# Kernel optimization log

Measured on AMD Instinct MI355X. Metric: run time of the kernel, lower is better.

The kernel has to match this reference:

```python
import jax, jax.numpy as jnp
import numpy as np

NUM_HEADS = 12


def _rel_indices(H, W):
    # [N, N, 3] with channels (dx, dy, dx^2+dy^2), N = H*W
    indx = jnp.arange(W)[None, :] - jnp.arange(W)[:, None]          # [W, W]
    indx = jnp.tile(indx, (H, H))                                    # [N, N]
    indy = jnp.arange(H)[None, :] - jnp.arange(H)[:, None]          # [H, H]
    indy = jnp.repeat(jnp.repeat(indy, W, axis=0), W, axis=1)        # [N, N]
    indd = indx ** 2 + indy ** 2
    return jnp.stack([indx, indy, indd], axis=-1).astype(jnp.float32)


def setup_inputs() -> dict:
    key = jax.random.key(0)
    ks = jax.random.split(key, 8)
    B, N, C = 16, 576, 768
    std = 0.02
    return {
        "x": jax.random.normal(ks[0], (B, N, C), dtype=jnp.float32),
        "Wq": jax.random.normal(ks[1], (C, C), dtype=jnp.float32) * std,
        "Wk": jax.random.normal(ks[2], (C, C), dtype=jnp.float32) * std,
        "Wv": jax.random.normal(ks[3], (C, C), dtype=jnp.float32) * std,
        "Wproj": jax.random.normal(ks[4], (C, C), dtype=jnp.float32) * std,
        "bproj": jnp.zeros((C,), dtype=jnp.float32),
        "pos_w": jax.random.normal(ks[5], (3, NUM_HEADS), dtype=jnp.float32) * std,
        "pos_b": jnp.zeros((NUM_HEADS,), dtype=jnp.float32),
        "gating": jnp.ones((NUM_HEADS,), dtype=jnp.float32),
        "H": 24,
        "W": 24,
    }


def reference(x, Wq, Wk, Wv, Wproj, bproj, pos_w, pos_b, gating, H, W):
    B, N, C = x.shape
    h = gating.shape[0]
    d = C // h
    scale = d ** (-0.5)

    def heads(t):  # [B,N,C] -> [B,h,N,d]
        return t.reshape(B, N, h, d).transpose(0, 2, 1, 3)

    q = heads(x @ Wq)
    k = heads(x @ Wk)
    v = heads(x @ Wv)

    # content scores: [B,h,N,N]
    patch_score = jax.nn.softmax(jnp.einsum('bhnd,bhmd->bhnm', q, k) * scale, axis=-1)

    # positional scores: shared across batch, [h,N,N]
    rel = _rel_indices(H, W)                      # [N,N,3]
    pos_score = jnp.einsum('nmc,ch->hnm', rel, pos_w) + pos_b[:, None, None]
    pos_score = jax.nn.softmax(pos_score, axis=-1)

    gate = jax.nn.sigmoid(gating)[None, :, None, None]  # [1,h,1,1]
    attn = (1.0 - gate) * patch_score + gate * pos_score[None]
    attn = attn / jnp.sum(attn, axis=-1, keepdims=True)

    out = jnp.einsum('bhnm,bhmd->bhnd', attn, v)         # [B,h,N,d]
    out = out.transpose(0, 2, 1, 3).reshape(B, N, C)
    return out @ Wproj + bproj
```

## Files before the change

### kernel.cpp

```cpp
#include <hip/hip_runtime.h>
#include <math.h>

#define B_ 16
#define N_ 576
#define C_ 768
#define NH 12
#define D_ 64
#define GW 24
#define STR 68
#define QKV 2304

typedef unsigned short u16;
typedef __bf16 bf16x8 __attribute__((ext_vector_type(8)));
typedef float f32x4 __attribute__((ext_vector_type(4)));

__device__ __forceinline__ u16 f2bf(float f) {
    unsigned u = __builtin_bit_cast(unsigned, f);
    unsigned r = (u + 0x7FFFu + ((u >> 16) & 1u)) >> 16;
    return (u16)r;
}
__device__ __forceinline__ float bf2f(u16 b) {
    unsigned u = ((unsigned)b) << 16;
    return __builtin_bit_cast(float, u);
}

__device__ __forceinline__ bf16x8 ldsF8u(const u16* p) {
    union { uint2 u[2]; bf16x8 v; } t;
    t.u[0] = *(const uint2*)p;
    t.u[1] = *(const uint2*)(p + 4);
    return t.v;
}
__device__ __forceinline__ bf16x8 ldsF8a(const u16* p) {
    union { uint4 u; bf16x8 v; } t;
    t.u = *(const uint4*)p;
    return t.v;
}

__device__ __forceinline__ void gload16(const u16* g, u16* l) {
    __builtin_amdgcn_global_load_lds(
        (const __attribute__((address_space(1))) void*)g,
        (__attribute__((address_space(3))) void*)l,
        16, 0, 0);
}

__global__ __launch_bounds__(256)
void conv_x_kernel(const float* __restrict__ x, u16* __restrict__ xb)
{
    int i = blockIdx.x * 256 + threadIdx.x;
    float4 v = ((const float4*)x)[i];
    u16 o[4] = {f2bf(v.x), f2bf(v.y), f2bf(v.z), f2bf(v.w)};
    *(uint2*)&xb[(size_t)i * 4] = *(const uint2*)o;
}

__global__ __launch_bounds__(256)
void transpose_w4_kernel(const float* __restrict__ w0, const float* __restrict__ w1,
                         const float* __restrict__ w2, const float* __restrict__ w3,
                         u16* __restrict__ dst_base)
{
    const float* srcs[4] = {w0, w1, w2, w3};
    const float* src = srcs[blockIdx.z];
    u16* dst = dst_base + (size_t)blockIdx.z * C_ * C_;
    __shared__ float t[32][33];
    const int bx = blockIdx.x * 32, by = blockIdx.y * 32;
    const int tx = threadIdx.x & 31, ty = threadIdx.x >> 5;
#pragma unroll
    for (int i = 0; i < 32; i += 8)
        t[ty + i][tx] = src[(size_t)(by + ty + i) * C_ + bx + tx];
    __syncthreads();
#pragma unroll
    for (int i = 0; i < 32; i += 8)
        dst[(size_t)(bx + ty + i) * C_ + by + tx] = f2bf(t[tx][ty + i]);
}

__global__ __launch_bounds__(256)
void transpose_v_kernel(const u16* __restrict__ qkvb, u16* __restrict__ vtb)
{
    __shared__ u16 t[64 * 72];
    const int n0 = blockIdx.x * 64;
    const int bh = blockIdx.y;
    const int b = bh / NH, h = bh % NH;
    const int tid = threadIdx.x;
    const u16* src = qkvb + ((size_t)b * N_ + n0) * QKV + 2 * C_ + h * D_;
#pragma unroll
    for (int p = 0; p < 2; ++p) {
        int idx = p * 256 + tid;
        int r = idx >> 3, c = (idx & 7) << 3;
        *(uint4*)&t[r * 72 + c] = *(const uint4*)(src + (size_t)r * QKV + c);
    }
    __syncthreads();
    u16* dst = vtb + (size_t)bh * D_ * N_ + n0;
#pragma unroll
    for (int p = 0; p < 2; ++p) {
        int idx = p * 256 + tid;
        int dd = idx >> 3, n8 = (idx & 7) << 3;
        u16 o[8];
#pragma unroll
        for (int j = 0; j < 8; ++j) o[j] = t[(n8 + j) * 72 + dd];
        *(uint4*)(dst + (size_t)dd * N_ + n8) = *(const uint4*)o;
    }
}

__global__ __launch_bounds__(256)
void mfma_gemm(const u16* __restrict__ A,
               const u16* __restrict__ BT,
               const float* __restrict__ bias,
               float* __restrict__ out,
               u16* __restrict__ outb,
               int ldo, int mode)
{
    const int K = C_;
    __shared__ __align__(16) u16 As[128 * 64];
    __shared__ __align__(16) u16 Bs[128 * 64];
    const int tid = threadIdx.x;
    const int wave = tid >> 6, lane = tid & 63;
    const int quad = lane >> 4, l16 = lane & 15;
    const int wy = wave >> 1, wx = wave & 1;
    const int tm = blockIdx.y * 128, tn = blockIdx.x * 128;

    const int lr = lane >> 3;
    const int sc = ((lane & 7) ^ lr) * 8;

    f32x4 acc[4][4];
#pragma unroll
    for (int i = 0; i < 4; ++i)
#pragma unroll
        for (int j = 0; j < 4; ++j)
            acc[i][j] = (f32x4){0.f, 0.f, 0.f, 0.f};

    for (int k0 = 0; k0 < K; k0 += 64) {
        __syncthreads();
#pragma unroll
        for (int t = 0; t < 4; ++t) {
            const int rg = wave * 32 + t * 8;
            gload16(A  + (size_t)(tm + rg + lr) * K + k0 + sc, &As[rg * 64]);
            gload16(BT + (size_t)(tn + rg + lr) * K + k0 + sc, &Bs[rg * 64]);
        }
        __syncthreads();

#pragma unroll
        for (int kh = 0; kh < 2; ++kh) {
            bf16x8 aA[4], bB[4];
#pragma unroll
            for (int i = 0; i < 4; ++i) {
                const int s = (kh * 4 + quad) ^ (l16 & 7);
                aA[i] = ldsF8a(&As[(wy * 64 + i * 16 + l16) * 64 + s * 8]);
            }
#pragma unroll
            for (int j = 0; j < 4; ++j) {
                const int s = (kh * 4 + quad) ^ (l16 & 7);
                bB[j] = ldsF8a(&Bs[(wx * 64 + j * 16 + l16) * 64 + s * 8]);
            }
#pragma unroll
            for (int i = 0; i < 4; ++i)
#pragma unroll
                for (int j = 0; j < 4; ++j)
                    acc[i][j] = __builtin_amdgcn_mfma_f32_16x16x32_bf16(aA[i], bB[j], acc[i][j], 0, 0, 0);
        }
    }

    if (mode == 0) {
#pragma unroll
        for (int i = 0; i < 4; ++i) {
#pragma unroll
            for (int r = 0; r < 4; ++r) {
                const int m = tm + wy * 64 + i * 16 + quad * 4 + r;
#pragma unroll
                for (int j = 0; j < 4; ++j) {
                    const int c = tn + wx * 64 + j * 16 + l16;
                    out[(size_t)m * ldo + c] = acc[i][j][r] + bias[c];
                }
            }
        }
    } else {
        const float scale = (tn < C_) ? 0.125f : 1.0f;
#pragma unroll
        for (int i = 0; i < 4; ++i) {
#pragma unroll
            for (int r = 0; r < 4; ++r) {
                const int m = tm + wy * 64 + i * 16 + quad * 4 + r;
#pragma unroll
                for (int j = 0; j < 4; ++j) {
                    const int c = tn + wx * 64 + j * 16 + l16;
                    outb[(size_t)m * ldo + c] = f2bf(acc[i][j][r] * scale);
                }
            }
        }
    }
}

__global__ __launch_bounds__(256)
void pos_stage1_kernel(const u16* __restrict__ qkvb,
                       const float* __restrict__ pos_w,
                       float* __restrict__ T1)
{
    const int bh = blockIdx.x;
    const int b = bh / NH, h = bh % NH;
    const int tid = threadIdx.x;
    __shared__ float ey[47];
    const float w1 = pos_w[NH + h], w2 = pos_w[2 * NH + h];

    if (tid < 47) {
        float dy = (float)(tid - 23);
        ey[tid] = __expf(w1 * dy + w2 * dy * dy);
    }
    __syncthreads();
    if (tid >= 192) return;
    const int mx = tid >> 3, c = (tid & 7) << 3;
    const u16* src = qkvb + (size_t)b * N_ * QKV + 2 * C_ + h * D_ + c;

#pragma unroll
    for (int np = 0; np < 3; ++np) {
        float acc[8][8];
#pragma unroll
        for (int q = 0; q < 8; ++q)
#pragma unroll
            for (int j = 0; j < 8; ++j) acc[q][j] = 0.f;
        for (int my = 0; my < GW; ++my) {
            union { uint4 u; u16 s[8]; } d;
            d.u = *(const uint4*)(src + (size_t)(my * GW + mx) * QKV);
            float vf[8];
#pragma unroll
            for (int j = 0; j < 8; ++j) vf[j] = bf2f(d.s[j]);
#pragma unroll
            for (int q = 0; q < 8; ++q) {
                float e = ey[my - (np * 8 + q) + 23];
#pragma unroll
                for (int j = 0; j < 8; ++j) acc[q][j] += e * vf[j];
            }
        }
#pragma unroll
        for (int q = 0; q < 8; ++q) {
            const int ny = np * 8 + q;
            float* dst = T1 + (((size_t)bh * GW + ny) * GW + mx) * D_ + c;
            *(float4*)dst       = *(float4*)&acc[q][0];
            *(float4*)(dst + 4) = *(float4*)&acc[q][4];
        }
    }
}

__global__ __launch_bounds__(256)
void pos_stage2_kernel(const float* __restrict__ T1,
                       const float* __restrict__ pos_w,
                       const float* __restrict__ gating,
                       u16* __restrict__ aob)
{
    const int bh = blockIdx.x;
    const int ny = blockIdx.y;
    const int b = bh / NH, h = bh % NH;
    const int tid = threadIdx.x;
    __shared__ float T1s[GW * D_];
    __shared__ float ex[47];
    __shared__ float SxA[GW];
    __shared__ float Sy;
    const float w0 = pos_w[h], w1 = pos_w[NH + h], w2 = pos_w[2 * NH + h];

    const float* tsrc = T1 + ((size_t)bh * GW + ny) * GW * D_;
#pragma unroll
    for (int i = 0; i < 2; ++i) {
        int idx = i * 256 + tid;
        if (idx < 384) ((float4*)T1s)[idx] = ((const float4*)tsrc)[idx];
    }
    if (tid < 47) {
        float dx = (float)(tid - 23);
        ex[tid] = __expf(w0 * dx + w2 * dx * dx);
    }
    if (tid == 192) {
        float s = 0.f;
        for (int my = 0; my < GW; ++my) {
            float dy = (float)(my - ny);
            s += __expf(w1 * dy + w2 * dy * dy);
        }
        Sy = s;
    }
    __syncthreads();
    if (tid < GW) {
        float s = 0.f;
        for (int mx = 0; mx < GW; ++mx) s += ex[mx - tid + 23];
        SxA[tid] = s;
    }
    __syncthreads();
    if (tid >= 192) return;
    const int nx = tid >> 3, c = (tid & 7) << 3;

    float acc[8];
#pragma unroll
    for (int j = 0; j < 8; ++j) acc[j] = 0.f;
    for (int mx = 0; mx < GW; ++mx) {
        float e = ex[mx - nx + 23];
        float4 t0 = *(float4*)&T1s[mx * D_ + c];
        float4 t1 = *(float4*)&T1s[mx * D_ + c + 4];
        acc[0] += e * t0.x; acc[1] += e * t0.y; acc[2] += e * t0.z; acc[3] += e * t0.w;
        acc[4] += e * t1.x; acc[5] += e * t1.y; acc[6] += e * t1.z; acc[7] += e * t1.w;
    }
    const float g = 1.f / (1.f + __expf(-gating[h]));
    const float sc = g / (SxA[nx] * Sy);
    const int n = ny * GW + nx;
    u16* dst = aob + ((size_t)b * N_ + n) * C_ + h * D_ + c;
    u16 cur[8];
    *(uint4*)cur = *(const uint4*)dst;
    u16 o[8];
#pragma unroll
    for (int j = 0; j < 8; ++j) o[j] = f2bf(bf2f(cur[j]) + sc * acc[j]);
    *(uint4*)dst = *(const uint4*)o;
}

__global__ __launch_bounds__(256)
void attn_kernel(const u16* __restrict__ qkvb,
                 const u16* __restrict__ vt,
                 const float* __restrict__ gating,
                 u16* __restrict__ ao)
{
    const int qt = blockIdx.x;
    const int bh = blockIdx.y;
    const int b = bh / NH, h = bh % NH;
    const int tid = threadIdx.x;
    const int wave = tid >> 6, lane = tid & 63;
    const int quad = lane >> 4, l16 = lane & 15;

    __shared__ u16 smem[3 * 64 * STR];
    u16* Kt = smem;
    u16* Vs = smem + 64 * STR;
    u16* Pb = smem + 2 * 64 * STR;

    const u16* qptr  = qkvb + ((size_t)b * N_ + qt * 64) * QKV + h * D_;
    const u16* kbase = qkvb + (size_t)b * N_ * QKV + C_ + h * D_;
    const u16* vbase = vt + (size_t)bh * D_ * N_;

    const int sr = tid >> 3;
    const int scol = (tid & 7) << 3;

#pragma unroll
    for (int p = 0; p < 2; ++p) {
        int r = p * 32 + sr;
        uint4 d = *(const uint4*)(qptr + (size_t)r * QKV + scol);
        *(uint2*)&Pb[r * STR + scol]     = make_uint2(d.x, d.y);
        *(uint2*)&Pb[r * STR + scol + 4] = make_uint2(d.z, d.w);
    }
    __syncthreads();

    const int arow = wave * 16 + l16;
    bf16x8 aq0 = ldsF8u(&Pb[arow * STR + quad * 8]);
    bf16x8 aq1 = ldsF8u(&Pb[arow * STR + 32 + quad * 8]);

    uint4 rk[2], rv[2];
    auto loadT = [&](int m0) {
#pragma unroll
        for (int p = 0; p < 2; ++p) {
            int r = p * 32 + sr;
            rk[p] = *(const uint4*)(kbase + (size_t)(m0 + r) * QKV + scol);
            rv[p] = *(const uint4*)(vbase + (size_t)r * N_ + m0 + scol);
        }
    };
    auto writeT = [&]() {
#pragma unroll
        for (int p = 0; p < 2; ++p) {
            int r = p * 32 + sr;
            *(uint2*)&Kt[r * STR + scol]     = make_uint2(rk[p].x, rk[p].y);
            *(uint2*)&Kt[r * STR + scol + 4] = make_uint2(rk[p].z, rk[p].w);
            *(uint2*)&Vs[r * STR + scol]     = make_uint2(rv[p].x, rv[p].y);
            *(uint2*)&Vs[r * STR + scol + 4] = make_uint2(rv[p].z, rv[p].w);
        }
    };

    loadT(0);

    f32x4 oc[4];
#pragma unroll
    for (int nt = 0; nt < 4; ++nt)
        oc[nt] = (f32x4){0.f, 0.f, 0.f, 0.f};
    float lrun[4] = {0.f, 0.f, 0.f, 0.f};

    for (int mt = 0; mt < 9; ++mt) {
        __syncthreads();
        writeT();
        __syncthreads();
        if (mt < 8) loadT((mt + 1) * 64);

        f32x4 s[4];
#pragma unroll
        for (int nt = 0; nt < 4; ++nt) {
            bf16x8 b0 = ldsF8u(&Kt[(nt * 16 + l16) * STR + quad * 8]);
            bf16x8 b1 = ldsF8u(&Kt[(nt * 16 + l16) * STR + 32 + quad * 8]);
            f32x4 z = (f32x4){0.f, 0.f, 0.f, 0.f};
            z = __builtin_amdgcn_mfma_f32_16x16x32_bf16(aq0, b0, z, 0, 0, 0);
            z = __builtin_amdgcn_mfma_f32_16x16x32_bf16(aq1, b1, z, 0, 0, 0);
            s[nt] = z;
        }

#pragma unroll
        for (int r = 0; r < 4; ++r) {
            const int prow = (wave * 16 + quad * 4 + r) * STR;
            float e0 = __expf(s[0][r]);
            float e1 = __expf(s[1][r]);
            float e2 = __expf(s[2][r]);
            float e3 = __expf(s[3][r]);
            Pb[prow +  0 + l16] = f2bf(e0);
            Pb[prow + 16 + l16] = f2bf(e1);
            Pb[prow + 32 + l16] = f2bf(e2);
            Pb[prow + 48 + l16] = f2bf(e3);
            lrun[r] += (e0 + e1) + (e2 + e3);
        }
        asm volatile("s_waitcnt lgkmcnt(0)" ::: "memory");

#pragma unroll
        for (int ks = 0; ks < 2; ++ks) {
            bf16x8 ap = ldsF8u(&Pb[arow * STR + ks * 32 + quad * 8]);
#pragma unroll
            for (int nt = 0; nt < 4; ++nt) {
                bf16x8 bv = ldsF8u(&Vs[(nt * 16 + l16) * STR + ks * 32 + quad * 8]);
                oc[nt] = __builtin_amdgcn_mfma_f32_16x16x32_bf16(ap, bv, oc[nt], 0, 0, 0);
            }
        }
    }

#pragma unroll
    for (int r = 0; r < 4; ++r) {
        lrun[r] += __shfl_xor(lrun[r], 1, 64);
        lrun[r] += __shfl_xor(lrun[r], 2, 64);
        lrun[r] += __shfl_xor(lrun[r], 4, 64);
        lrun[r] += __shfl_xor(lrun[r], 8, 64);
    }

    const float g = 1.f / (1.f + __expf(-gating[h]));
#pragma unroll
    for (int r = 0; r < 4; ++r) {
        const float sc = (1.f - g) / lrun[r];
        const int row = qt * 64 + wave * 16 + quad * 4 + r;
#pragma unroll
        for (int nt = 0; nt < 4; ++nt) {
            ao[((size_t)b * N_ + row) * C_ + h * D_ + nt * 16 + l16] =
                f2bf(oc[nt][r] * sc);
        }
    }
}

extern "C" void kernel_launch(void* const* d_in, const int* in_sizes, int n_in,
                              void* d_out, int out_size, void* d_ws, size_t ws_size,
                              hipStream_t stream)
{
    const float* x      = (const float*)d_in[0];
    const float* Wq     = (const float*)d_in[1];
    const float* Wk     = (const float*)d_in[2];
    const float* Wv     = (const float*)d_in[3];
    const float* Wproj  = (const float*)d_in[4];
    const float* bproj  = (const float*)d_in[5];
    const float* pos_w  = (const float*)d_in[6];
    const float* gating = (const float*)d_in[8];
    float* out = (float*)d_out;

    const size_t xe = (size_t)B_ * N_ * C_;
    const size_t we = (size_t)C_ * C_;
    const size_t qe = (size_t)B_ * N_ * QKV;
    u16* xb   = (u16*)d_ws;
    u16* wt   = xb + xe;
    u16* qkvb = wt + 4 * we;
    u16* vtb  = qkvb + qe;
    u16* aob  = vtb + xe;
    float* T1 = (float*)(aob + xe);
    size_t need = (size_t)(3 * xe + 4 * we + qe) * sizeof(u16)
                + (size_t)B_ * NH * GW * GW * D_ * sizeof(float);
    if (ws_size < need) return;

    conv_x_kernel<<<dim3((unsigned)(xe / 1024)), 256, 0, stream>>>(x, xb);
    transpose_w4_kernel<<<dim3(24, 24, 4), 256, 0, stream>>>(Wq, Wk, Wv, Wproj, wt);

    mfma_gemm<<<dim3(18, 72), 256, 0, stream>>>(xb, wt, nullptr, nullptr,
                                                qkvb, QKV, 1);
    transpose_v_kernel<<<dim3(9, B_ * NH), 256, 0, stream>>>(qkvb, vtb);
    pos_stage1_kernel<<<dim3(B_ * NH), 256, 0, stream>>>(qkvb, pos_w, T1);
    attn_kernel<<<dim3(9, B_ * NH), 256, 0, stream>>>(qkvb, vtb, gating, aob);
    pos_stage2_kernel<<<dim3(B_ * NH, GW), 256, 0, stream>>>(T1, pos_w, gating, aob);
    mfma_gemm<<<dim3(6, 72), 256, 0, stream>>>(aob, wt + 3 * we, bproj, out,
                                               nullptr, C_, 0);
}
```

Before: 258.1 us.

## Merge prep and V-transpose kernels; vectorize GEMM epilogue via swapped MFMA operands

Folds the x-conversion and weight-transpose kernels into one launch, and the V-transpose and positional stage-1 kernels into another, so there are fewer launches and the independent work can run concurrently. Swaps the MFMA operands so each lane holds four consecutive columns. The fp32 epilogue then writes float4 stores with vector bias loads, and the bf16 epilogue stages through padded LDS for coalesced 16-byte row stores. This adds an extra LDS round-trip and barrier in the bf16 path, and makes the merged kernels heterogeneous.

```diff
diff --git a/kernel.cpp b/kernel.cpp
--- a/kernel.cpp
+++ b/kernel.cpp
@@ -9,6 +9,7 @@
 #define GW 24
 #define STR 68
 #define QKV 2304
+#define CSTR 136
 
 typedef unsigned short u16;
 typedef __bf16 bf16x8 __attribute__((ext_vector_type(8)));
@@ -44,25 +45,29 @@
 }
 
 __global__ __launch_bounds__(256)
-void conv_x_kernel(const float* __restrict__ x, u16* __restrict__ xb)
-{
-    int i = blockIdx.x * 256 + threadIdx.x;
-    float4 v = ((const float4*)x)[i];
-    u16 o[4] = {f2bf(v.x), f2bf(v.y), f2bf(v.z), f2bf(v.w)};
-    *(uint2*)&xb[(size_t)i * 4] = *(const uint2*)o;
-}
-
-__global__ __launch_bounds__(256)
-void transpose_w4_kernel(const float* __restrict__ w0, const float* __restrict__ w1,
-                         const float* __restrict__ w2, const float* __restrict__ w3,
-                         u16* __restrict__ dst_base)
-{
+void prep_kernel(const float* __restrict__ x,
+                 const float* __restrict__ w0, const float* __restrict__ w1,
+                 const float* __restrict__ w2, const float* __restrict__ w3,
+                 u16* __restrict__ xb, u16* __restrict__ wt_base)
+{
+    const int tid = threadIdx.x;
+    if (blockIdx.z == 4) {
+        const int flat = blockIdx.y * 24 + blockIdx.x;
+#pragma unroll
+        for (int it = 0; it < 12; ++it) {
+            int idx = flat * 3072 + it * 256 + tid;
+            float4 v = ((const float4*)x)[idx];
+            u16 o[4] = {f2bf(v.x), f2bf(v.y), f2bf(v.z), f2bf(v.w)};
+            *(uint2*)&xb[(size_t)idx * 4] = *(const uint2*)o;
+        }
+        return;
+    }
     const float* srcs[4] = {w0, w1, w2, w3};
     const float* src = srcs[blockIdx.z];
-    u16* dst = dst_base + (size_t)blockIdx.z * C_ * C_;
+    u16* dst = wt_base + (size_t)blockIdx.z * C_ * C_;
     __shared__ float t[32][33];
     const int bx = blockIdx.x * 32, by = blockIdx.y * 32;
-    const int tx = threadIdx.x & 31, ty = threadIdx.x >> 5;
+    const int tx = tid & 31, ty = tid >> 5;
 #pragma unroll
     for (int i = 0; i < 32; i += 8)
         t[ty + i][tx] = src[(size_t)(by + ty + i) * C_ + bx + tx];
@@ -70,34 +75,6 @@
 #pragma unroll
     for (int i = 0; i < 32; i += 8)
         dst[(size_t)(bx + ty + i) * C_ + by + tx] = f2bf(t[tx][ty + i]);
-}
-
-__global__ __launch_bounds__(256)
-void transpose_v_kernel(const u16* __restrict__ qkvb, u16* __restrict__ vtb)
-{
-    __shared__ u16 t[64 * 72];
-    const int n0 = blockIdx.x * 64;
-    const int bh = blockIdx.y;
-    const int b = bh / NH, h = bh % NH;
-    const int tid = threadIdx.x;
-    const u16* src = qkvb + ((size_t)b * N_ + n0) * QKV + 2 * C_ + h * D_;
-#pragma unroll
-    for (int p = 0; p < 2; ++p) {
-        int idx = p * 256 + tid;
-        int r = idx >> 3, c = (idx & 7) << 3;
-        *(uint4*)&t[r * 72 + c] = *(const uint4*)(src + (size_t)r * QKV + c);
-    }
-    __syncthreads();
-    u16* dst = vtb + (size_t)bh * D_ * N_ + n0;
-#pragma unroll
-    for (int p = 0; p < 2; ++p) {
-        int idx = p * 256 + tid;
-        int dd = idx >> 3, n8 = (idx & 7) << 3;
-        u16 o[8];
-#pragma unroll
-        for (int j = 0; j < 8; ++j) o[j] = t[(n8 + j) * 72 + dd];
-        *(uint4*)(dst + (size_t)dd * N_ + n8) = *(const uint4*)o;
-    }
 }
 
 __global__ __launch_bounds__(256)
@@ -109,8 +86,9 @@
                int ldo, int mode)
 {
     const int K = C_;
-    __shared__ __align__(16) u16 As[128 * 64];
-    __shared__ __align__(16) u16 Bs[128 * 64];
+    __shared__ __align__(16) u16 smem[128 * CSTR];
+    u16* As = smem;
+    u16* Bs = smem + 128 * 64;
     const int tid = threadIdx.x;
     const int wave = tid >> 6, lane = tid & 63;
     const int quad = lane >> 4, l16 = lane & 15;
@@ -154,51 +132,91 @@
             for (int i = 0; i < 4; ++i)
 #pragma unroll
                 for (int j = 0; j < 4; ++j)
-                    acc[i][j] = __builtin_amdgcn_mfma_f32_16x16x32_bf16(aA[i], bB[j], acc[i][j], 0, 0, 0);
+                    acc[i][j] = __builtin_amdgcn_mfma_f32_16x16x32_bf16(bB[j], aA[i], acc[i][j], 0, 0, 0);
         }
     }
 
     if (mode == 0) {
 #pragma unroll
         for (int i = 0; i < 4; ++i) {
-#pragma unroll
-            for (int r = 0; r < 4; ++r) {
-                const int m = tm + wy * 64 + i * 16 + quad * 4 + r;
-#pragma unroll
-                for (int j = 0; j < 4; ++j) {
-                    const int c = tn + wx * 64 + j * 16 + l16;
-                    out[(size_t)m * ldo + c] = acc[i][j][r] + bias[c];
-                }
+            const int m = tm + wy * 64 + i * 16 + l16;
+#pragma unroll
+            for (int j = 0; j < 4; ++j) {
+                const int c = tn + wx * 64 + j * 16 + quad * 4;
+                float4 bv = *(const float4*)&bias[c];
+                float4 o;
+                o.x = acc[i][j][0] + bv.x;
+                o.y = acc[i][j][1] + bv.y;
+                o.z = acc[i][j][2] + bv.z;
+                o.w = acc[i][j][3] + bv.w;
+                *(float4*)&out[(size_t)m * ldo + c] = o;
             }
         }
     } else {
         const float scale = (tn < C_) ? 0.125f : 1.0f;
+        __syncthreads();
 #pragma unroll
         for (int i = 0; i < 4; ++i) {
-#pragma unroll
-            for (int r = 0; r < 4; ++r) {
-                const int m = tm + wy * 64 + i * 16 + quad * 4 + r;
-#pragma unroll
-                for (int j = 0; j < 4; ++j) {
-                    const int c = tn + wx * 64 + j * 16 + l16;
-                    outb[(size_t)m * ldo + c] = f2bf(acc[i][j][r] * scale);
-                }
-            }
+            const int ml = wy * 64 + i * 16 + l16;
+#pragma unroll
+            for (int j = 0; j < 4; ++j) {
+                const int cl = wx * 64 + j * 16 + quad * 4;
+                u16 o[4];
+#pragma unroll
+                for (int r = 0; r < 4; ++r) o[r] = f2bf(acc[i][j][r] * scale);
+                *(uint2*)&smem[ml * CSTR + cl] = *(const uint2*)o;
+            }
+        }
+        __syncthreads();
+#pragma unroll
+        for (int p = 0; p < 2; ++p) {
+            const int idx = p * 256 + tid;
+            const int row = idx >> 2, qq = idx & 3;
+            const u16* srcl = &smem[row * CSTR + qq * 32];
+            u16* dstg = outb + (size_t)(tm + row) * ldo + tn + qq * 32;
+#pragma unroll
+            for (int t = 0; t < 4; ++t)
+                *(uint4*)(dstg + t * 8) = *(const uint4*)(srcl + t * 8);
         }
     }
 }
 
 __global__ __launch_bounds__(256)
-void pos_stage1_kernel(const u16* __restrict__ qkvb,
-                       const float* __restrict__ pos_w,
-                       float* __restrict__ T1)
-{
-    const int bh = blockIdx.x;
+void tv_pos1_kernel(const u16* __restrict__ qkvb,
+                    const float* __restrict__ pos_w,
+                    u16* __restrict__ vtb,
+                    float* __restrict__ T1)
+{
+    const int bh = blockIdx.y;
     const int b = bh / NH, h = bh % NH;
     const int tid = threadIdx.x;
+
+    if (blockIdx.x < 9) {
+        __shared__ u16 t[64 * 72];
+        const int n0 = blockIdx.x * 64;
+        const u16* src = qkvb + ((size_t)b * N_ + n0) * QKV + 2 * C_ + h * D_;
+#pragma unroll
+        for (int p = 0; p < 2; ++p) {
+            int idx = p * 256 + tid;
+            int r = idx >> 3, c = (idx & 7) << 3;
+            *(uint4*)&t[r * 72 + c] = *(const uint4*)(src + (size_t)r * QKV + c);
+        }
+        __syncthreads();
+        u16* dst = vtb + (size_t)bh * D_ * N_ + n0;
+#pragma unroll
+        for (int p = 0; p < 2; ++p) {
+            int idx = p * 256 + tid;
+            int dd = idx >> 3, n8 = (idx & 7) << 3;
+            u16 o[8];
+#pragma unroll
+            for (int j = 0; j < 8; ++j) o[j] = t[(n8 + j) * 72 + dd];
+            *(uint4*)(dst + (size_t)dd * N_ + n8) = *(const uint4*)o;
+        }
+        return;
+    }
+
     __shared__ float ey[47];
     const float w1 = pos_w[NH + h], w2 = pos_w[2 * NH + h];
-
     if (tid < 47) {
         float dy = (float)(tid - 23);
         ey[tid] = __expf(w1 * dy + w2 * dy * dy);
@@ -461,13 +479,11 @@
                 + (size_t)B_ * NH * GW * GW * D_ * sizeof(float);
     if (ws_size < need) return;
 
-    conv_x_kernel<<<dim3((unsigned)(xe / 1024)), 256, 0, stream>>>(x, xb);
-    transpose_w4_kernel<<<dim3(24, 24, 4), 256, 0, stream>>>(Wq, Wk, Wv, Wproj, wt);
+    prep_kernel<<<dim3(24, 24, 5), 256, 0, stream>>>(x, Wq, Wk, Wv, Wproj, xb, wt);
 
     mfma_gemm<<<dim3(18, 72), 256, 0, stream>>>(xb, wt, nullptr, nullptr,
                                                 qkvb, QKV, 1);
-    transpose_v_kernel<<<dim3(9, B_ * NH), 256, 0, stream>>>(qkvb, vtb);
-    pos_stage1_kernel<<<dim3(B_ * NH), 256, 0, stream>>>(qkvb, pos_w, T1);
+    tv_pos1_kernel<<<dim3(10, B_ * NH), 256, 0, stream>>>(qkvb, pos_w, vtb, T1);
     attn_kernel<<<dim3(9, B_ * NH), 256, 0, stream>>>(qkvb, vtb, gating, aob);
     pos_stage2_kernel<<<dim3(B_ * NH, GW), 256, 0, stream>>>(T1, pos_w, gating, aob);
     mfma_gemm<<<dim3(6, 72), 256, 0, stream>>>(aob, wt + 3 * we, bproj, out,
```

Result: slower. 274.2 us (+6.2%).
